# Kernel optimization log

Measured on AMD Instinct MI355X. Metric: run time of the kernel, lower is better.

Reference implementation:

```python
import jax, jax.numpy as jnp
import numpy as np
import math

L, D, NH, HD, H, V = 6, 384, 6, 64, 768, 4096
B, T = 4, 2048


def setup_inputs() -> dict:
    key = jax.random.key(0)
    ks = jax.random.split(key, 16)
    s = 0.02
    inp = {
        "x": jax.random.randint(ks[0], (B, T), 0, V, dtype=jnp.int32),
        "emb": jax.random.normal(ks[1], (V, D), jnp.float32) * s,
        "wq": jax.random.normal(ks[2], (L, D, D), jnp.float32) * s,
        "wk": jax.random.normal(ks[3], (L, D, D), jnp.float32) * s,
        "wv": jax.random.normal(ks[4], (L, D, D), jnp.float32) * s,
        "wo": jax.random.normal(ks[5], (L, D, D), jnp.float32) * s,
        "ln1": jnp.ones((L, D), jnp.float32),
        "ln2": jnp.ones((L, D), jnp.float32),
        "w1": jax.random.normal(ks[6], (L, D, H), jnp.float32) * s,
        "b1": jnp.zeros((L, H), jnp.float32),
        "w2": jax.random.normal(ks[7], (L, H, D), jnp.float32) * s,
        "b2": jnp.zeros((L, D), jnp.float32),
        "lnf": jnp.ones((D,), jnp.float32),
        "head": jax.random.normal(ks[8], (D, V), jnp.float32) * s,
    }
    return inp


def _rms(x, w):
    return x * jax.lax.rsqrt(jnp.mean(x * x, axis=-1, keepdims=True) + 1e-6) * w


def _attn(x, wq, wk, wv, wo):
    b, t, _ = x.shape
    q = (x @ wq).reshape(b, t, NH, HD).transpose(0, 2, 1, 3)  # [b,h,t,hd]
    k = (x @ wk).reshape(b, t, NH, HD).transpose(0, 2, 1, 3)
    v = (x @ wv).reshape(b, t, NH, HD).transpose(0, 2, 1, 3)
    scores = jnp.einsum('bhqd,bhkd->bhqk', q, k) / math.sqrt(HD)
    causal = jnp.tril(jnp.ones((t, t), bool))
    scores = jnp.where(causal, scores, -jnp.inf)
    a = jax.nn.softmax(scores, axis=-1)
    o = jnp.einsum('bhqk,bhkd->bhqd', a, v)
    o = o.transpose(0, 2, 1, 3).reshape(b, t, D)
    return o @ wo


def reference(x, emb, wq, wk, wv, wo, ln1, ln2, w1, b1, w2, b2, lnf, head):
    h = emb[x]  # [B,T,D]
    mid = None
    for i in range(L):
        h = h + _attn(_rms(h, ln1[i]), wq[i], wk[i], wv[i], wo[i])
        hn = _rms(h, ln2[i])
        ff = jax.nn.gelu(hn @ w1[i] + b1[i], approximate=False) @ w2[i] + b2[i]
        h = h + ff
        if i == 2:
            mid = h
    logits = _rms(h, lnf) @ head
    return logits, mid
```

## Files before the change

kernel.cpp:

```cpp
#include <hip/hip_runtime.h>
#include <hip/hip_bf16.h>
#include <math.h>

#define L_  6
#define D_  384
#define NH_ 6
#define HD_ 64
#define HF_ 768
#define V_  4096
#define B_  4
#define T_  2048
#define BT_ (B_*T_)

typedef unsigned short u16;
typedef __attribute__((ext_vector_type(8))) short short8;
typedef __attribute__((ext_vector_type(4))) float f32x4;

__device__ __forceinline__ float bf2f(u16 u){
  union { unsigned int i; float f; } c; c.i = ((unsigned int)u)<<16; return c.f;
}
__device__ __forceinline__ u16 f2bf(float f){
  union { float f; unsigned int i; } c; c.f = f;
  unsigned int x = c.i;
  x += 0x7fffu + ((x>>16)&1u);
  return (u16)(x>>16);
}
__device__ __forceinline__ f32x4 mfma16(short8 a, short8 b, f32x4 c){
  return __builtin_amdgcn_mfma_f32_16x16x32_bf16(a,b,c,0,0,0);
}
template<int CTRL>
__device__ __forceinline__ float dppmax(float x){
  int v = __builtin_amdgcn_update_dpp(0, __builtin_bit_cast(int, x), CTRL, 0xf, 0xf, true);
  return fmaxf(x, __builtin_bit_cast(float, v));
}
__device__ __forceinline__ float rowmax16(float x){
  x = dppmax<0xB1>(x);
  x = dppmax<0x4E>(x);
  x = dppmax<0x141>(x);
  x = dppmax<0x140>(x);
  return x;
}
#define GLD16(gp, lp) __builtin_amdgcn_global_load_lds( \
    (const __attribute__((address_space(1))) void*)(gp), \
    (__attribute__((address_space(3))) void*)(lp), 16, 0, 0)

__global__ void embed_kernel(const int* __restrict__ x, const float* __restrict__ emb,
                             float* __restrict__ h){
  const int idx = blockIdx.x*256 + threadIdx.x;
  if(idx >= BT_*D_) return;
  const int t = idx / D_;
  const int d = idx - t*D_;
  h[idx] = emb[(size_t)x[t]*D_ + d];
}

__global__ __launch_bounds__(256) void wtrans_kernel(const float* __restrict__ src,
    u16* __restrict__ dst, int K, int N, size_t srcBatch, size_t dstBatch){
  __shared__ float tile[32][33];
  src += (size_t)blockIdx.z*srcBatch;
  dst += (size_t)blockIdx.z*dstBatch;
  const int tx = threadIdx.x&31, ty = threadIdx.x>>5;
  const int n0 = blockIdx.x*32, k0 = blockIdx.y*32;
  #pragma unroll
  for(int j=0;j<4;j++)
    tile[ty+j*8][tx] = src[(size_t)(k0+ty+j*8)*N + n0+tx];
  __syncthreads();
  #pragma unroll
  for(int j=0;j<4;j++)
    dst[(size_t)(n0+ty+j*8)*K + k0+tx] = f2bf(tile[tx][ty+j*8]);
}

__global__ __launch_bounds__(256) void rms_kernel(const float* __restrict__ h,
                                                  const float* __restrict__ w,
                                                  u16* __restrict__ out){
  const int wave = threadIdx.x>>6, lane = threadIdx.x&63;
  const size_t row = (size_t)blockIdx.x*4 + wave;
  const float* hr = h + row*D_;
  float v[6]; float ss = 0.f;
  #pragma unroll
  for(int i=0;i<6;i++){ v[i] = hr[lane + i*64]; ss += v[i]*v[i]; }
  #pragma unroll
  for(int o=1;o<64;o<<=1) ss += __shfl_xor(ss, o);
  const float rn = rsqrtf(ss*(1.f/D_) + 1e-6f);
  u16* orow = out + row*D_;
  #pragma unroll
  for(int i=0;i<6;i++) orow[lane+i*64] = f2bf(v[i]*rn*w[lane+i*64]);
}

__global__ void copy_kernel(const float* __restrict__ src, float* __restrict__ dst, int n){
  const int i = blockIdx.x*256 + threadIdx.x;
  if(i < n) dst[i] = src[i];
}

template<int MODE, int K, int BN>
__global__ __launch_bounds__(256) void gemm_kernel(
    const u16* __restrict__ A, const u16* __restrict__ Wt, int N,
    const float* __restrict__ bias, u16* __restrict__ out, float* __restrict__ fout,
    u16* __restrict__ qo, u16* __restrict__ ko, u16* __restrict__ vo)
{
  __shared__ u16 As[2][128*64];
  __shared__ u16 Bs[2][BN*64];
  const int w = threadIdx.x>>6, lane = threadIdx.x&63;
  const int l16 = lane&15, quad = lane>>4;
  const int r0 = blockIdx.y*128, n0 = blockIdx.x*BN;
  const int mst = lane>>3;
  const int cst = (lane&7) ^ (lane>>3);

  constexpr int MI = (BN==128) ? 4 : 2;
  constexpr int NKT = K/64;
  const int wrow = (BN==128) ? (w&1)*64 : w*32;
  const int wcol = (BN==128) ? (w>>1)*64 : 0;

  f32x4 acc[MI][4];
  #pragma unroll
  for(int mi=0;mi<MI;mi++)
    #pragma unroll
    for(int ni=0;ni<4;ni++){ acc[mi][ni][0]=0.f; acc[mi][ni][1]=0.f; acc[mi][ni][2]=0.f; acc[mi][ni][3]=0.f; }

  auto stage = [&](int kt, int bu){
    const int k0 = kt*64;
    #pragma unroll
    for(int i=0;i<4;i++){
      const int m = (w*4+i)*8 + mst;
      GLD16(A + (size_t)(r0+m)*K + k0 + cst*8, &As[bu][(w*4+i)*512]);
    }
    if constexpr(BN==128){
      #pragma unroll
      for(int i=0;i<4;i++){
        const int n = (w*4+i)*8 + mst;
        GLD16(Wt + (size_t)(n0+n)*K + k0 + cst*8, &Bs[bu][(w*4+i)*512]);
      }
    } else {
      #pragma unroll
      for(int i=0;i<2;i++){
        const int n = (w*2+i)*8 + mst;
        GLD16(Wt + (size_t)(n0+n)*K + k0 + cst*8, &Bs[bu][(w*2+i)*512]);
      }
    }
  };

  stage(0, 0);
  for(int kt=0; kt<NKT; kt++){
    const u16* Ac = As[kt&1];
    const u16* Bc = Bs[kt&1];
    if(kt+1 < NKT){
      stage(kt+1, (kt+1)&1);
      if constexpr(BN==128) asm volatile("s_waitcnt vmcnt(8)" ::: "memory");
      else                  asm volatile("s_waitcnt vmcnt(6)" ::: "memory");
    } else {
      asm volatile("s_waitcnt vmcnt(0)" ::: "memory");
    }
    __builtin_amdgcn_s_barrier();
    asm volatile("" ::: "memory");

    __builtin_amdgcn_s_setprio(1);
    #pragma unroll
    for(int ks=0;ks<2;ks++){
      short8 av[MI], bv[4];
      #pragma unroll
      for(int mi=0;mi<MI;mi++){
        const int m = wrow + mi*16 + l16;
        av[mi] = *(const short8*)&Ac[m*64 + (((ks*4+quad)^(l16&7))*8)];
      }
      #pragma unroll
      for(int ni=0;ni<4;ni++){
        const int n = wcol + ni*16 + l16;
        bv[ni] = *(const short8*)&Bc[n*64 + (((ks*4+quad)^(l16&7))*8)];
      }
      #pragma unroll
      for(int mi=0;mi<MI;mi++)
        #pragma unroll
        for(int ni=0;ni<4;ni++)
          acc[mi][ni] = mfma16(av[mi], bv[ni], acc[mi][ni]);
    }
    __builtin_amdgcn_s_setprio(0);
    if(kt+1 < NKT){
      asm volatile("" ::: "memory");
      __builtin_amdgcn_s_barrier();
    }
  }

  #pragma unroll
  for(int mi=0;mi<MI;mi++){
    #pragma unroll
    for(int ni=0;ni<4;ni++){
      const int col = n0 + wcol + ni*16 + l16;
      #pragma unroll
      for(int r=0;r<4;r++){
        const int row = r0 + wrow + mi*16 + quad*4 + r;
        float v = acc[mi][ni][r];
        if(MODE==0){
          fout[(size_t)row*N + col] = v;
        } else if(MODE==1){
          v += bias[col];
          v = 0.5f*v*(1.f + erff(v*0.70710678118f));
          out[(size_t)row*N + col] = f2bf(v);
        } else if(MODE==2){
          if(bias) v += bias[col];
          fout[(size_t)row*N + col] += v;
        } else {
          if(col < D_)        qo[(size_t)row*D_ + col]      = f2bf(v);
          else if(col < 2*D_) ko[(size_t)row*D_ + (col-D_)] = f2bf(v);
          else {
            const int cv = col - 2*D_;
            const int hh = cv>>6, dd = cv&63;
            const int bb = row>>11, tt = row&(T_-1);
            vo[(((size_t)(bb*NH_+hh))*HD_ + dd)*T_ + tt] = f2bf(v);
          }
        }
      }
    }
  }
}

__global__ __launch_bounds__(256) void flash_kernel(const u16* __restrict__ q,
    const u16* __restrict__ k, const u16* __restrict__ vt, u16* __restrict__ ao){
  __shared__ u16 Ks[2][64*64];
  __shared__ u16 Vs[2][80*64];
  __shared__ __align__(16) u16 Pb[4][16*64];
  const int tid = threadIdx.x;
  const int w = tid>>6, lane = tid&63;
  const int l16 = lane&15, quad = lane>>4;
  const int bh = blockIdx.y, b = bh/NH_, h = bh - b*NH_;
  const int qt = (gridDim.x-1) - blockIdx.x;
  const int qw = qt*64 + w*16;

  {
    const int idx0 = tid*8;
    #pragma unroll
    for(int i=0;i<8;i++){
      const int idx = idx0 + i;
      const int bu = idx>>10, rem = idx&1023;
      Vs[bu][(64 + (rem>>6))*64 + (rem&63)] = ((rem>>6)==0) ? (u16)0x3F80 : (u16)0;
    }
  }
  __syncthreads();

  const u16* qp = q + ((size_t)(b*T_ + qw + l16))*D_ + h*HD_ + quad*8;
  short8 qf0 = *(const short8*)(qp);
  short8 qf1 = *(const short8*)(qp + 32);

  const u16* kbase = k + (size_t)(b*T_)*D_ + h*HD_;
  const u16* vbase = vt + (size_t)(b*NH_ + h)*HD_*T_;
  u16* Pw = &Pb[w][0];

  const int srow = lane>>3;
  const int schunk = lane&7;
  const int kgc = schunk ^ srow;

  float m[4];
  f32x4 o[5];
  #pragma unroll
  for(int r=0;r<4;r++) m[r] = -1e30f;
  #pragma unroll
  for(int c=0;c<5;c++){ o[c][0]=0.f; o[c][1]=0.f; o[c][2]=0.f; o[c][3]=0.f; }

  const int nkt = qt + 1;

  #pragma unroll
  for(int i=0;i<2;i++){
    const int j = w*2+i;
    GLD16(kbase + (size_t)(j*8 + srow)*D_ + kgc*8, &Ks[0][j*512]);
  }
  #pragma unroll
  for(int i=0;i<2;i++){
    const int j = w*2+i;
    GLD16(vbase + (size_t)(j*8 + srow)*T_ + (schunk^srow)*8, &Vs[0][j*512]);
  }

  for(int kt=0; kt<nkt; kt++){
    const u16* Kc = Ks[kt&1];
    const u16* Vc = Vs[kt&1];
    if(kt+1 < nkt){
      const int kb2 = (kt+1)*64;
      #pragma unroll
      for(int i=0;i<2;i++){
        const int j = w*2+i;
        GLD16(kbase + (size_t)(kb2 + j*8 + srow)*D_ + kgc*8, &Ks[(kt+1)&1][j*512]);
      }
      #pragma unroll
      for(int i=0;i<2;i++){
        const int j = w*2+i;
        GLD16(vbase + (size_t)(j*8 + srow)*T_ + kb2 + (schunk^srow)*8, &Vs[(kt+1)&1][j*512]);
      }
      asm volatile("s_waitcnt vmcnt(4)" ::: "memory");
    } else {
      asm volatile("s_waitcnt vmcnt(0)" ::: "memory");
    }
    __builtin_amdgcn_s_barrier();

    float s[4][4];
    __builtin_amdgcn_s_setprio(1);
    #pragma unroll
    for(int c=0;c<4;c++){
      const int krow = c*16 + l16;
      short8 kf0 = *(const short8*)&Kc[krow*64 + ((quad^(l16&7))*8)];
      short8 kf1 = *(const short8*)&Kc[krow*64 + (((4+quad)^(l16&7))*8)];
      f32x4 sa = {0.f,0.f,0.f,0.f};
      sa = mfma16(qf0, kf0, sa);
      sa = mfma16(qf1, kf1, sa);
      #pragma unroll
      for(int r=0;r<4;r++) s[c][r] = sa[r]*0.125f;
    }
    __builtin_amdgcn_s_setprio(0);
    if(kt == nkt-1){
      const int kb = kt*64;
      #pragma unroll
      for(int c=0;c<4;c++){
        const int kpos = kb + c*16 + l16;
        #pragma unroll
        for(int r=0;r<4;r++)
          if(kpos > qw + quad*4 + r) s[c][r] = -1e30f;
      }
    }
    float tmr[4];
    #pragma unroll
    for(int r=0;r<4;r++){
      float tm = fmaxf(fmaxf(s[0][r], s[1][r]), fmaxf(s[2][r], s[3][r]));
      tmr[r] = rowmax16(tm);
    }
    float need = tmr[0] - m[0];
    #pragma unroll
    for(int r=1;r<4;r++) need = fmaxf(need, tmr[r] - m[r]);
    if(!__all(need <= 8.f)){
      #pragma unroll
      for(int r=0;r<4;r++){
        const float mn = fmaxf(m[r], tmr[r]);
        const float al = __expf(m[r] - mn);
        #pragma unroll
        for(int c=0;c<5;c++) o[c][r] *= al;
        m[r] = mn;
      }
    }
    #pragma unroll
    for(int r=0;r<4;r++){
      const int prow = quad*4 + r;
      #pragma unroll
      for(int c=0;c<4;c++){
        const float p = __expf(s[c][r] - m[r]);
        Pw[prow*64 + (((c*2 + (l16>>3)) ^ (prow&7))<<3) + (l16&7)] = f2bf(p);
      }
    }
    __builtin_amdgcn_s_setprio(1);
    #pragma unroll
    for(int kk=0;kk<2;kk++){
      short8 pf = *(const short8*)&Pw[l16*64 + (((kk*4+quad) ^ (l16&7))<<3)];
      #pragma unroll
      for(int c=0;c<5;c++){
        const int dd = c*16 + l16;
        short8 vf = *(const short8*)&Vc[dd*64 + (((kk*4+quad)^(l16&7))<<3)];
        o[c] = mfma16(pf, vf, o[c]);
      }
    }
    __builtin_amdgcn_s_setprio(0);
    __builtin_amdgcn_s_barrier();
  }
  #pragma unroll
  for(int r=0;r<4;r++){
    const float lr = __shfl(o[4][r], quad<<4, 64);
    const float il = 1.f / lr;
    const size_t row = (size_t)(b*T_ + qw + quad*4 + r);
    #pragma unroll
    for(int c=0;c<4;c++)
      ao[row*D_ + h*HD_ + c*16 + l16] = f2bf(o[c][r] * il);
  }
}

extern "C" void kernel_launch(void* const* d_in, const int* in_sizes, int n_in,
                              void* d_out, int out_size, void* d_ws, size_t ws_size,
                              hipStream_t stream) {
  const int*   x    = (const int*)d_in[0];
  const float* emb  = (const float*)d_in[1];
  const float* wq   = (const float*)d_in[2];
  const float* wk   = (const float*)d_in[3];
  const float* wv   = (const float*)d_in[4];
  const float* wo   = (const float*)d_in[5];
  const float* ln1  = (const float*)d_in[6];
  const float* ln2  = (const float*)d_in[7];
  const float* w1   = (const float*)d_in[8];
  const float* b1   = (const float*)d_in[9];
  const float* w2   = (const float*)d_in[10];
  const float* b2   = (const float*)d_in[11];
  const float* lnf  = (const float*)d_in[12];
  const float* head = (const float*)d_in[13];
  float* out = (float*)d_out;

  char* ws = (char*)d_ws; size_t off = 0;
  auto alloc = [&](size_t bytes)->void* {
    void* p = ws + off; off += (bytes + 255) & ~(size_t)255; return p;
  };
  float* hbuf  = (float*)alloc((size_t)BT_*D_*4);
  u16* xn    = (u16*)alloc((size_t)BT_*D_*2);
  u16* qb    = (u16*)alloc((size_t)BT_*D_*2);
  u16* kb    = (u16*)alloc((size_t)BT_*D_*2);
  u16* vtb   = (u16*)alloc((size_t)BT_*D_*2);
  u16* aob   = (u16*)alloc((size_t)BT_*D_*2);
  u16* midb  = (u16*)alloc((size_t)BT_*HF_*2);
  u16* qkvt  = (u16*)alloc((size_t)L_*3*D_*D_*2);
  u16* wot   = (u16*)alloc((size_t)L_*D_*D_*2);
  u16* w1t   = (u16*)alloc((size_t)L_*HF_*D_*2);
  u16* w2t   = (u16*)alloc((size_t)L_*D_*HF_*2);
  u16* headt = (u16*)alloc((size_t)V_*D_*2);

  const dim3 blk(256);
  wtrans_kernel<<<dim3(D_/32, D_/32, L_), blk, 0, stream>>>(wq, qkvt,           D_, D_, (size_t)D_*D_, (size_t)3*D_*D_);
  wtrans_kernel<<<dim3(D_/32, D_/32, L_), blk, 0, stream>>>(wk, qkvt + D_*D_,   D_, D_, (size_t)D_*D_, (size_t)3*D_*D_);
  wtrans_kernel<<<dim3(D_/32, D_/32, L_), blk, 0, stream>>>(wv, qkvt + 2*D_*D_, D_, D_, (size_t)D_*D_, (size_t)3*D_*D_);
  wtrans_kernel<<<dim3(D_/32, D_/32, L_), blk, 0, stream>>>(wo, wot,            D_, D_, (size_t)D_*D_, (size_t)D_*D_);
  wtrans_kernel<<<dim3(HF_/32, D_/32, L_), blk, 0, stream>>>(w1, w1t, D_, HF_, (size_t)D_*HF_, (size_t)HF_*D_);
  wtrans_kernel<<<dim3(D_/32, HF_/32, L_), blk, 0, stream>>>(w2, w2t, HF_, D_, (size_t)D_*HF_, (size_t)D_*HF_);
  wtrans_kernel<<<dim3(V_/32, D_/32, 1),  blk, 0, stream>>>(head, headt, D_, V_, 0, 0);

  embed_kernel<<<(BT_*D_ + 255)/256, blk, 0, stream>>>(x, emb, hbuf);

  for(int li=0; li<L_; li++){
    rms_kernel<<<BT_/4, blk, 0, stream>>>(hbuf, ln1 + li*D_, xn);
    gemm_kernel<3,D_,128><<<dim3(3*D_/128, BT_/128), blk, 0, stream>>>(
        xn, qkvt + (size_t)li*3*D_*D_, 3*D_, nullptr, nullptr, nullptr, qb, kb, vtb);
    flash_kernel<<<dim3(T_/64, B_*NH_), blk, 0, stream>>>(qb, kb, vtb, aob);
    gemm_kernel<2,D_,64><<<dim3(D_/64, BT_/128), blk, 0, stream>>>(
        aob, wot + (size_t)li*D_*D_, D_, nullptr, nullptr, hbuf, nullptr, nullptr, nullptr);
    rms_kernel<<<BT_/4, blk, 0, stream>>>(hbuf, ln2 + li*D_, xn);
    gemm_kernel<1,D_,128><<<dim3(HF_/128, BT_/128), blk, 0, stream>>>(
        xn, w1t + (size_t)li*HF_*D_, HF_, b1 + li*HF_, midb, nullptr, nullptr, nullptr, nullptr);
    gemm_kernel<2,HF_,64><<<dim3(D_/64, BT_/128), blk, 0, stream>>>(
        midb, w2t + (size_t)li*D_*HF_, D_, b2 + li*D_, nullptr, hbuf, nullptr, nullptr, nullptr);
    if(li == 2)
      copy_kernel<<<(BT_*D_ + 255)/256, blk, 0, stream>>>(hbuf, out + (size_t)BT_*V_, BT_*D_);
  }
  rms_kernel<<<BT_/4, blk, 0, stream>>>(hbuf, lnf, xn);
  gemm_kernel<0,D_,128><<<dim3(V_/128, BT_/128), blk, 0, stream>>>(
      xn, headt, V_, nullptr, nullptr, out, nullptr, nullptr, nullptr);
}
```

Before: 1.205 ms.

## Enlarge flash attention Q tile to 128 rows and fuse mid-copy into FFN2 GEMM

The flash attention kernel now gives each wave 32 query rows (two 16-row groups) instead of 16, so each block covers 128 queries. Every K/V tile loaded into shared memory is reused across twice as many MFMAs, and K/V traffic per query drops. The grid halves, which lowers occupancy and parallelism, and tiles that lie fully above the causal diagonal for a wave are skipped. Separately, the layer-2 FFN down-projection now writes the residual to both hbuf and the mid output, which removes the standalone copy kernel.

```diff
diff --git a/kernel.cpp b/kernel.cpp
--- a/kernel.cpp
+++ b/kernel.cpp
@@ -86,16 +86,12 @@
   for(int i=0;i<6;i++) orow[lane+i*64] = f2bf(v[i]*rn*w[lane+i*64]);
 }
 
-__global__ void copy_kernel(const float* __restrict__ src, float* __restrict__ dst, int n){
-  const int i = blockIdx.x*256 + threadIdx.x;
-  if(i < n) dst[i] = src[i];
-}
-
 template<int MODE, int K, int BN>
 __global__ __launch_bounds__(256) void gemm_kernel(
     const u16* __restrict__ A, const u16* __restrict__ Wt, int N,
     const float* __restrict__ bias, u16* __restrict__ out, float* __restrict__ fout,
-    u16* __restrict__ qo, u16* __restrict__ ko, u16* __restrict__ vo)
+    u16* __restrict__ qo, u16* __restrict__ ko, u16* __restrict__ vo,
+    float* __restrict__ fout2)
 {
   __shared__ u16 As[2][128*64];
   __shared__ u16 Bs[2][BN*64];
@@ -197,6 +193,11 @@
         } else if(MODE==2){
           if(bias) v += bias[col];
           fout[(size_t)row*N + col] += v;
+        } else if(MODE==4){
+          v += bias[col];
+          const float nv = fout[(size_t)row*N + col] + v;
+          fout[(size_t)row*N + col] = nv;
+          fout2[(size_t)row*N + col] = nv;
         } else {
           if(col < D_)        qo[(size_t)row*D_ + col]      = f2bf(v);
           else if(col < 2*D_) ko[(size_t)row*D_ + (col-D_)] = f2bf(v);
@@ -216,13 +217,13 @@
     const u16* __restrict__ k, const u16* __restrict__ vt, u16* __restrict__ ao){
   __shared__ u16 Ks[2][64*64];
   __shared__ u16 Vs[2][80*64];
-  __shared__ __align__(16) u16 Pb[4][16*64];
+  __shared__ __align__(16) u16 Pb[4][32*64];
   const int tid = threadIdx.x;
   const int w = tid>>6, lane = tid&63;
   const int l16 = lane&15, quad = lane>>4;
   const int bh = blockIdx.y, b = bh/NH_, h = bh - b*NH_;
   const int qt = (gridDim.x-1) - blockIdx.x;
-  const int qw = qt*64 + w*16;
+  const int qw = qt*128 + w*32;
 
   {
     const int idx0 = tid*8;
@@ -235,9 +236,13 @@
   }
   __syncthreads();
 
-  const u16* qp = q + ((size_t)(b*T_ + qw + l16))*D_ + h*HD_ + quad*8;
-  short8 qf0 = *(const short8*)(qp);
-  short8 qf1 = *(const short8*)(qp + 32);
+  short8 qf[2][2];
+  #pragma unroll
+  for(int rg=0;rg<2;rg++){
+    const u16* qp = q + ((size_t)(b*T_ + qw + rg*16 + l16))*D_ + h*HD_ + quad*8;
+    qf[rg][0] = *(const short8*)(qp);
+    qf[rg][1] = *(const short8*)(qp + 32);
+  }
 
   const u16* kbase = k + (size_t)(b*T_)*D_ + h*HD_;
   const u16* vbase = vt + (size_t)(b*NH_ + h)*HD_*T_;
@@ -247,14 +252,17 @@
   const int schunk = lane&7;
   const int kgc = schunk ^ srow;
 
-  float m[4];
-  f32x4 o[5];
-  #pragma unroll
-  for(int r=0;r<4;r++) m[r] = -1e30f;
-  #pragma unroll
-  for(int c=0;c<5;c++){ o[c][0]=0.f; o[c][1]=0.f; o[c][2]=0.f; o[c][3]=0.f; }
-
-  const int nkt = qt + 1;
+  float m[2][4];
+  f32x4 o[2][5];
+  #pragma unroll
+  for(int rg=0;rg<2;rg++){
+    #pragma unroll
+    for(int r=0;r<4;r++) m[rg][r] = -1e30f;
+    #pragma unroll
+    for(int c=0;c<5;c++){ o[rg][c][0]=0.f; o[rg][c][1]=0.f; o[rg][c][2]=0.f; o[rg][c][3]=0.f; }
+  }
+
+  const int nkt = 2*qt + 2;
 
   #pragma unroll
   for(int i=0;i<2;i++){
@@ -288,81 +296,103 @@
     }
     __builtin_amdgcn_s_barrier();
 
-    float s[4][4];
-    __builtin_amdgcn_s_setprio(1);
-    #pragma unroll
-    for(int c=0;c<4;c++){
-      const int krow = c*16 + l16;
-      short8 kf0 = *(const short8*)&Kc[krow*64 + ((quad^(l16&7))*8)];
-      short8 kf1 = *(const short8*)&Kc[krow*64 + (((4+quad)^(l16&7))*8)];
-      f32x4 sa = {0.f,0.f,0.f,0.f};
-      sa = mfma16(qf0, kf0, sa);
-      sa = mfma16(qf1, kf1, sa);
-      #pragma unroll
-      for(int r=0;r<4;r++) s[c][r] = sa[r]*0.125f;
-    }
-    __builtin_amdgcn_s_setprio(0);
-    if(kt == nkt-1){
-      const int kb = kt*64;
+    const int kb = kt*64;
+    if(kb <= qw + 31){
+      float s[2][4][4];
+      __builtin_amdgcn_s_setprio(1);
       #pragma unroll
       for(int c=0;c<4;c++){
-        const int kpos = kb + c*16 + l16;
-        #pragma unroll
-        for(int r=0;r<4;r++)
-          if(kpos > qw + quad*4 + r) s[c][r] = -1e30f;
-      }
-    }
-    float tmr[4];
+        const int krow = c*16 + l16;
+        short8 kf0 = *(const short8*)&Kc[krow*64 + ((quad^(l16&7))*8)];
+        short8 kf1 = *(const short8*)&Kc[krow*64 + (((4+quad)^(l16&7))*8)];
+        #pragma unroll
+        for(int rg=0;rg<2;rg++){
+          f32x4 sa = {0.f,0.f,0.f,0.f};
+          sa = mfma16(qf[rg][0], kf0, sa);
+          sa = mfma16(qf[rg][1], kf1, sa);
+          #pragma unroll
+          for(int r=0;r<4;r++) s[rg][c][r] = sa[r]*0.125f;
+        }
+      }
+      __builtin_amdgcn_s_setprio(0);
+      if(kb + 63 > qw){
+        #pragma unroll
+        for(int rg=0;rg<2;rg++)
+          #pragma unroll
+          for(int c=0;c<4;c++){
+            const int kpos = kb + c*16 + l16;
+            #pragma unroll
+            for(int r=0;r<4;r++)
+              if(kpos > qw + rg*16 + quad*4 + r) s[rg][c][r] = -1e30f;
+          }
+      }
+      float tmr[2][4];
+      #pragma unroll
+      for(int rg=0;rg<2;rg++)
+        #pragma unroll
+        for(int r=0;r<4;r++){
+          float tm = fmaxf(fmaxf(s[rg][0][r], s[rg][1][r]), fmaxf(s[rg][2][r], s[rg][3][r]));
+          tmr[rg][r] = rowmax16(tm);
+        }
+      float need = -1e30f;
+      #pragma unroll
+      for(int rg=0;rg<2;rg++)
+        #pragma unroll
+        for(int r=0;r<4;r++) need = fmaxf(need, tmr[rg][r] - m[rg][r]);
+      if(!__all(need <= 8.f)){
+        #pragma unroll
+        for(int rg=0;rg<2;rg++)
+          #pragma unroll
+          for(int r=0;r<4;r++){
+            const float mn = fmaxf(m[rg][r], tmr[rg][r]);
+            const float al = __expf(m[rg][r] - mn);
+            #pragma unroll
+            for(int c=0;c<5;c++) o[rg][c][r] *= al;
+            m[rg][r] = mn;
+          }
+      }
+      #pragma unroll
+      for(int rg=0;rg<2;rg++)
+        #pragma unroll
+        for(int r=0;r<4;r++){
+          const int prow = rg*16 + quad*4 + r;
+          #pragma unroll
+          for(int c=0;c<4;c++){
+            const float p = __expf(s[rg][c][r] - m[rg][r]);
+            Pw[prow*64 + (((c*2 + (l16>>3)) ^ (prow&7))<<3) + (l16&7)] = f2bf(p);
+          }
+        }
+      __builtin_amdgcn_s_setprio(1);
+      #pragma unroll
+      for(int kk=0;kk<2;kk++){
+        short8 pf[2];
+        #pragma unroll
+        for(int rg=0;rg<2;rg++)
+          pf[rg] = *(const short8*)&Pw[(rg*16 + l16)*64 + (((kk*4+quad) ^ (l16&7))<<3)];
+        #pragma unroll
+        for(int c=0;c<5;c++){
+          const int dd = c*16 + l16;
+          short8 vf = *(const short8*)&Vc[dd*64 + (((kk*4+quad)^(l16&7))<<3)];
+          #pragma unroll
+          for(int rg=0;rg<2;rg++)
+            o[rg][c] = mfma16(pf[rg], vf, o[rg][c]);
+        }
+      }
+      __builtin_amdgcn_s_setprio(0);
+    }
+    __builtin_amdgcn_s_barrier();
+  }
+  #pragma unroll
+  for(int rg=0;rg<2;rg++)
     #pragma unroll
     for(int r=0;r<4;r++){
-      float tm = fmaxf(fmaxf(s[0][r], s[1][r]), fmaxf(s[2][r], s[3][r]));
-      tmr[r] = rowmax16(tm);
-    }
-    float need = tmr[0] - m[0];
-    #pragma unroll
-    for(int r=1;r<4;r++) need = fmaxf(need, tmr[r] - m[r]);
-    if(!__all(need <= 8.f)){
-      #pragma unroll
-      for(int r=0;r<4;r++){
-        const float mn = fmaxf(m[r], tmr[r]);
-        const float al = __expf(m[r] - mn);
-        #pragma unroll
-        for(int c=0;c<5;c++) o[c][r] *= al;
-        m[r] = mn;
-      }
-    }
-    #pragma unroll
-    for(int r=0;r<4;r++){
-      const int prow = quad*4 + r;
-      #pragma unroll
-      for(int c=0;c<4;c++){
-        const float p = __expf(s[c][r] - m[r]);
-        Pw[prow*64 + (((c*2 + (l16>>3)) ^ (prow&7))<<3) + (l16&7)] = f2bf(p);
-      }
-    }
-    __builtin_amdgcn_s_setprio(1);
-    #pragma unroll
-    for(int kk=0;kk<2;kk++){
-      short8 pf = *(const short8*)&Pw[l16*64 + (((kk*4+quad) ^ (l16&7))<<3)];
-      #pragma unroll
-      for(int c=0;c<5;c++){
-        const int dd = c*16 + l16;
-        short8 vf = *(const short8*)&Vc[dd*64 + (((kk*4+quad)^(l16&7))<<3)];
-        o[c] = mfma16(pf, vf, o[c]);
-      }
-    }
-    __builtin_amdgcn_s_setprio(0);
-    __builtin_amdgcn_s_barrier();
-  }
-  #pragma unroll
-  for(int r=0;r<4;r++){
-    const float lr = __shfl(o[4][r], quad<<4, 64);
-    const float il = 1.f / lr;
-    const size_t row = (size_t)(b*T_ + qw + quad*4 + r);
-    #pragma unroll
-    for(int c=0;c<4;c++)
-      ao[row*D_ + h*HD_ + c*16 + l16] = f2bf(o[c][r] * il);
-  }
+      const float lr = __shfl(o[rg][4][r], quad<<4, 64);
+      const float il = 1.f / lr;
+      const size_t row = (size_t)(b*T_ + qw + rg*16 + quad*4 + r);
+      #pragma unroll
+      for(int c=0;c<4;c++)
+        ao[row*D_ + h*HD_ + c*16 + l16] = f2bf(o[rg][c][r] * il);
+    }
 }
 
 extern "C" void kernel_launch(void* const* d_in, const int* in_sizes, int n_in,
@@ -415,19 +445,22 @@
   for(int li=0; li<L_; li++){
     rms_kernel<<<BT_/4, blk, 0, stream>>>(hbuf, ln1 + li*D_, xn);
     gemm_kernel<3,D_,128><<<dim3(3*D_/128, BT_/128), blk, 0, stream>>>(
-        xn, qkvt + (size_t)li*3*D_*D_, 3*D_, nullptr, nullptr, nullptr, qb, kb, vtb);
-    flash_kernel<<<dim3(T_/64, B_*NH_), blk, 0, stream>>>(qb, kb, vtb, aob);
+        xn, qkvt + (size_t)li*3*D_*D_, 3*D_, nullptr, nullptr, nullptr, qb, kb, vtb, nullptr);
+    flash_kernel<<<dim3(T_/128, B_*NH_), blk, 0, stream>>>(qb, kb, vtb, aob);
     gemm_kernel<2,D_,64><<<dim3(D_/64, BT_/128), blk, 0, stream>>>(
-        aob, wot + (size_t)li*D_*D_, D_, nullptr, nullptr, hbuf, nullptr, nullptr, nullptr);
+        aob, wot + (size_t)li*D_*D_, D_, nullptr, nullptr, hbuf, nullptr, nullptr, nullptr, nullptr);
     rms_kernel<<<BT_/4, blk, 0, stream>>>(hbuf, ln2 + li*D_, xn);
     gemm_kernel<1,D_,128><<<dim3(HF_/128, BT_/128), blk, 0, stream>>>(
-        xn, w1t + (size_t)li*HF_*D_, HF_, b1 + li*HF_, midb, nullptr, nullptr, nullptr, nullptr);
-    gemm_kernel<2,HF_,64><<<dim3(D_/64, BT_/128), blk, 0, stream>>>(
-        midb, w2t + (size_t)li*D_*HF_, D_, b2 + li*D_, nullptr, hbuf, nullptr, nullptr, nullptr);
+        xn, w1t + (size_t)li*HF_*D_, HF_, b1 + li*HF_, midb, nullptr, nullptr, nullptr, nullptr, nullptr);
     if(li == 2)
-      copy_kernel<<<(BT_*D_ + 255)/256, blk, 0, stream>>>(hbuf, out + (size_t)BT_*V_, BT_*D_);
+      gemm_kernel<4,HF_,64><<<dim3(D_/64, BT_/128), blk, 0, stream>>>(
+          midb, w2t + (size_t)li*D_*HF_, D_, b2 + li*D_, nullptr, hbuf, nullptr, nullptr, nullptr,
+          out + (size_t)BT_*V_);
+    else
+      gemm_kernel<2,HF_,64><<<dim3(D_/64, BT_/128), blk, 0, stream>>>(
+          midb, w2t + (size_t)li*D_*HF_, D_, b2 + li*D_, nullptr, hbuf, nullptr, nullptr, nullptr, nullptr);
   }
   rms_kernel<<<BT_/4, blk, 0, stream>>>(hbuf, lnf, xn);
   gemm_kernel<0,D_,128><<<dim3(V_/128, BT_/128), blk, 0, stream>>>(
-      xn, headt, V_, nullptr, nullptr, out, nullptr, nullptr, nullptr);
-}
+      xn, headt, V_, nullptr, nullptr, out, nullptr, nullptr, nullptr, nullptr);
+}
```

Result: slower. 1.314 ms (+9.0%).
